# Kernel tuning notes

Hardware: AMD Instinct MI355X
Metric: run time of the kernel (lower is better)

## Reference

```python
import jax, jax.numpy as jnp
import numpy as np

N = 50000          # nodes
E = 800000         # directed edges (before self-loops)
HID = 64           # hidden_dim
HEADS = 4          # conv1 heads
NUM_CLASSES = 16
SLOPE = 0.2        # PyG GATConv default negative_slope


def setup_inputs() -> dict:
    key = jax.random.key(0)
    ks = jax.random.split(key, 10)
    s1 = 1.0 / np.sqrt(HID)
    s2 = 1.0 / np.sqrt(HEADS * HID)
    return {
        "x": jax.random.normal(ks[0], (N, HID), jnp.float32),
        "edge_index": jax.random.randint(ks[1], (2, E), 0, N, dtype=jnp.int64),
        # conv1: GATConv(64 -> 64, heads=4, concat)
        "W1": jax.random.normal(ks[2], (HID, HEADS * HID), jnp.float32) * s1,
        "att_src1": jax.random.normal(ks[3], (HEADS, HID), jnp.float32) * s1,
        "att_dst1": jax.random.normal(ks[4], (HEADS, HID), jnp.float32) * s1,
        "b1": jnp.zeros((HEADS * HID,), jnp.float32),
        # conv2: GATConv(256 -> num_classes, heads=1, concat)
        "W2": jax.random.normal(ks[5], (HEADS * HID, NUM_CLASSES), jnp.float32) * s2,
        "att_src2": jax.random.normal(ks[6], (1, NUM_CLASSES), jnp.float32) * s2,
        "att_dst2": jax.random.normal(ks[7], (1, NUM_CLASSES), jnp.float32) * s2,
        "b2": jnp.zeros((NUM_CLASSES,), jnp.float32),
    }


def _gat_conv(x, src, dst, W, att_s, att_d, b, heads, out_dim):
    # x: [N, F_in]; src/dst: [E'] with self-loops (PyG add_self_loops=True)
    xh = (x @ W).reshape(-1, heads, out_dim)                 # [N, H, D]
    a_src = jnp.einsum('nhd,hd->nh', xh, att_s)              # [N, H]
    a_dst = jnp.einsum('nhd,hd->nh', xh, att_d)              # [N, H]
    e = a_src[src] + a_dst[dst]                              # [E', H]
    e = jnp.where(e > 0, e, SLOPE * e)                       # leaky_relu(0.2)
    # segment softmax over incoming edges of each dst node
    m = jax.lax.stop_gradient(jax.ops.segment_max(e, dst, num_segments=N))
    ex = jnp.exp(e - m[dst])
    denom = jax.ops.segment_sum(ex, dst, num_segments=N)
    alpha = ex / (denom[dst] + 1e-16)                        # [E', H]
    out = jax.ops.segment_sum(xh[src] * alpha[:, :, None], dst, num_segments=N)
    return out.reshape(N, heads * out_dim) + b


def reference(x, edge_index, W1, att_src1, att_dst1, b1, W2, att_src2, att_dst2, b2):
    loops = jnp.arange(N, dtype=edge_index.dtype)
    src = jnp.concatenate([edge_index[0], loops])
    dst = jnp.concatenate([edge_index[1], loops])
    h = _gat_conv(x, src, dst, W1, att_src1, att_dst1, b1, HEADS, HID)
    h = jax.nn.elu(h)
    # F.dropout(p=0.5, training=False) -> identity at inference
    h = _gat_conv(h, src, dst, W2, att_src2, att_dst2, b2, 1, NUM_CLASSES)
    return jax.nn.log_softmax(h, axis=1)
```

## Files before the change

kernel.cpp:

```cpp
#include <hip/hip_runtime.h>
#include <hip/hip_bf16.h>
#include <math.h>

#define N_NODES 50000
#define N_EDGES 800000
#define EP (N_EDGES + N_NODES)
#define HID 64
#define HEADS 4
#define F1 (HEADS * HID)
#define NC 16
#define SLOPE 0.2f
#define NRT 3125
#define GMB 2048
#define NT 49

typedef __attribute__((ext_vector_type(8))) short short8;
typedef __attribute__((ext_vector_type(4))) float f32x4;

__device__ __forceinline__ unsigned short bf16rn(float f) {
    unsigned u = __float_as_uint(f);
    return (unsigned short)((u + 0x7fffu + ((u >> 16) & 1u)) >> 16);
}
__device__ __forceinline__ float bf_lo(unsigned p) { return __uint_as_float(p << 16); }
__device__ __forceinline__ float bf_hi(unsigned p) { return __uint_as_float(p & 0xffff0000u); }

__device__ __forceinline__ void edge_sd(int e, const int* __restrict__ ei, int& s, int& d) {
    if (e < N_EDGES) { s = ei[e]; d = ei[N_EDGES + e]; }
    else             { s = e - N_EDGES; d = s; }
}

__global__ __launch_bounds__(1024) void k_scan_local(const int* __restrict__ cnt,
        int* __restrict__ lexcl, int* __restrict__ bsum) {
    __shared__ int wsum[16];
    int t = threadIdx.x, lane = t & 63, wid = t >> 6;
    int i = blockIdx.x * 1024 + t;
    int v = (i < N_NODES) ? cnt[i] : 0;
    int s = v;
#pragma unroll
    for (int off = 1; off < 64; off <<= 1) {
        int x = __shfl_up(s, off);
        if (lane >= off) s += x;
    }
    if (lane == 63) wsum[wid] = s;
    __syncthreads();
    if (t < 16) {
        int w = wsum[t];
#pragma unroll
        for (int off = 1; off < 16; off <<= 1) {
            int x = __shfl_up(w, off);
            if (t >= off) w += x;
        }
        wsum[t] = w;
    }
    __syncthreads();
    int waveoff = (wid == 0) ? 0 : wsum[wid - 1];
    int incl = s + waveoff;
    if (i < N_NODES) lexcl[i] = incl - v;
    if (t == 1023) bsum[blockIdx.x] = incl;
}

__global__ __launch_bounds__(256) void k_scan_add(int* __restrict__ row_start,
        const int* __restrict__ bsum, int* __restrict__ cursor) {
    __shared__ int sb[64];
    __shared__ int stot;
    int t = threadIdx.x;
    if (t < 64) {
        int v = (t < NT) ? bsum[t] : 0;
        int s = v;
#pragma unroll
        for (int off = 1; off < 64; off <<= 1) {
            int x = __shfl_up(s, off);
            if (t >= off) s += x;
        }
        sb[t] = s - v;
        if (t == 63) stot = s;
    }
    __syncthreads();
    int i = blockIdx.x * 256 + t;
    if (i < N_NODES) {
        int v = row_start[i] + sb[i >> 10];
        row_start[i] = v;
        cursor[i] = v;
    }
    if (i == 0) row_start[N_NODES] = stot;
}

__global__ void k_scatter(const int* __restrict__ ei, int* __restrict__ cursor,
                          int* __restrict__ esrc) {
    int e = blockIdx.x * blockDim.x + threadIdx.x;
    if (e >= EP) return;
    int s, d; edge_sd(e, ei, s, d);
    int p = atomicAdd(&cursor[d], 1);
    esrc[p] = s;
}

__global__ __launch_bounds__(256) void k_gemm1(
        const float* __restrict__ x, const float* __restrict__ W1,
        const float* __restrict__ att_s, const float* __restrict__ att_d,
        unsigned short* __restrict__ xh1b, float* __restrict__ a_src, float* __restrict__ a_dst,
        const int* __restrict__ ei, int* __restrict__ cnt) {
    __shared__ float xs[16][68];
    int t = threadIdx.x;
    for (int e = blockIdx.x * 256 + t; e < EP; e += 256 * GMB) {
        int s, d; edge_sd(e, ei, s, d);
        atomicAdd(&cnt[d], 1);
    }
    int w = t >> 6, l = t & 63;
    int lo16 = l & 15, kg = l >> 4;
    short8 bfrag[4][2];
#pragma unroll
    for (int ct = 0; ct < 4; ++ct)
#pragma unroll
        for (int kh = 0; kh < 2; ++kh) {
            const float* wp = W1 + (size_t)(kh * 32 + kg * 8) * F1 + (w * 64 + ct * 16 + lo16);
            short8 f;
#pragma unroll
            for (int i = 0; i < 8; ++i) f[i] = (short)bf16rn(wp[(size_t)i * F1]);
            bfrag[ct][kh] = f;
        }
    float asv[4], adv[4];
#pragma unroll
    for (int ct = 0; ct < 4; ++ct) {
        asv[ct] = att_s[w * 64 + ct * 16 + lo16];
        adv[ct] = att_d[w * 64 + ct * 16 + lo16];
    }
    int sr = t >> 4, sc = (t & 15) * 4;
    for (int rt = blockIdx.x; rt < NRT; rt += GMB) {
        __syncthreads();
        *(float4*)&xs[sr][sc] = *(const float4*)(x + (size_t)(rt * 16 + sr) * HID + sc);
        __syncthreads();
        short8 af[2];
#pragma unroll
        for (int kh = 0; kh < 2; ++kh) {
            const float* xp = &xs[lo16][kh * 32 + kg * 8];
            float4 u0 = *(const float4*)xp;
            float4 u1 = *(const float4*)(xp + 4);
            short8 f;
            f[0] = (short)bf16rn(u0.x); f[1] = (short)bf16rn(u0.y);
            f[2] = (short)bf16rn(u0.z); f[3] = (short)bf16rn(u0.w);
            f[4] = (short)bf16rn(u1.x); f[5] = (short)bf16rn(u1.y);
            f[6] = (short)bf16rn(u1.z); f[7] = (short)bf16rn(u1.w);
            af[kh] = f;
        }
        f32x4 acc[4];
#pragma unroll
        for (int ct = 0; ct < 4; ++ct) {
            acc[ct] = (f32x4){0.f, 0.f, 0.f, 0.f};
            acc[ct] = __builtin_amdgcn_mfma_f32_16x16x32_bf16(af[0], bfrag[ct][0], acc[ct], 0, 0, 0);
            acc[ct] = __builtin_amdgcn_mfma_f32_16x16x32_bf16(af[1], bfrag[ct][1], acc[ct], 0, 0, 0);
        }
#pragma unroll
        for (int reg = 0; reg < 4; ++reg) {
            int gr = rt * 16 + kg * 4 + reg;
#pragma unroll
            for (int ct = 0; ct < 4; ++ct)
                xh1b[(size_t)gr * F1 + w * 64 + ct * 16 + lo16] = bf16rn(acc[ct][reg]);
            float ps = acc[0][reg] * asv[0] + acc[1][reg] * asv[1]
                     + acc[2][reg] * asv[2] + acc[3][reg] * asv[3];
            float pd = acc[0][reg] * adv[0] + acc[1][reg] * adv[1]
                     + acc[2][reg] * adv[2] + acc[3][reg] * adv[3];
#pragma unroll
            for (int o = 1; o <= 8; o <<= 1) {
                ps += __shfl_xor(ps, o);
                pd += __shfl_xor(pd, o);
            }
            if (lo16 == 0) {
                a_src[gr * HEADS + w] = ps;
                a_dst[gr * HEADS + w] = pd;
            }
        }
    }
}

__global__ __launch_bounds__(256) void k_csr1(
        const int* __restrict__ row_start, const int* __restrict__ esrc,
        const float* __restrict__ a_src, const float* __restrict__ a_dst,
        const unsigned short* __restrict__ xh1b, const float* __restrict__ b1,
        const float* __restrict__ W2, const float* __restrict__ att_s2,
        const float* __restrict__ att_d2,
        unsigned short* __restrict__ xh2b, float* __restrict__ a_src2,
        float* __restrict__ a_dst2) {
    int w = threadIdx.x >> 6, l = threadIdx.x & 63;
    int d = blockIdx.x * 4 + w;
    if (d >= N_NODES) return;
    int base = row_start[d], deg = row_start[d + 1] - base;
    __shared__ int   ls[4][64];
    __shared__ float lal[4][4][68];
    int h = l >> 4, e16 = l & 15;
    int eoff = l >> 5, fl = l & 31, hf = fl >> 3;
    int* lsw = ls[w];
    float adh = a_dst[d * HEADS + h];
    float denl = 0.0f;
    float a0=0.f,a1=0.f,a2=0.f,a3=0.f,a4=0.f,a5=0.f,a6=0.f,a7=0.f;
    for (int c0 = 0; c0 < deg; c0 += 64) {
        int cn = min(64, deg - c0);
        if (l < cn) lsw[l] = esrc[base + c0 + l];
        for (int j = e16; j < cn; j += 16) {
            float ev = a_src[lsw[j] * HEADS + h] + adh;
            ev = ev > 0.0f ? ev : SLOPE * ev;
            float wj = __expf(ev);
            lal[w][h][j] = wj;
            denl += wj;
        }
        const float* lalh = lal[w][hf];
        int j = 0;
        for (; j + 3 < cn; j += 4) {
            float wa = lalh[j + eoff], wb = lalh[j + 2 + eoff];
            uint4 pa = *(const uint4*)(xh1b + (size_t)lsw[j + eoff]     * F1 + 8 * fl);
            uint4 pb = *(const uint4*)(xh1b + (size_t)lsw[j + 2 + eoff] * F1 + 8 * fl);
            a0 += wa * bf_lo(pa.x); a1 += wa * bf_hi(pa.x);
            a2 += wa * bf_lo(pa.y); a3 += wa * bf_hi(pa.y);
            a4 += wa * bf_lo(pa.z); a5 += wa * bf_hi(pa.z);
            a6 += wa * bf_lo(pa.w); a7 += wa * bf_hi(pa.w);
            a0 += wb * bf_lo(pb.x); a1 += wb * bf_hi(pb.x);
            a2 += wb * bf_lo(pb.y); a3 += wb * bf_hi(pb.y);
            a4 += wb * bf_lo(pb.z); a5 += wb * bf_hi(pb.z);
            a6 += wb * bf_lo(pb.w); a7 += wb * bf_hi(pb.w);
        }
        for (; j + 1 < cn; j += 2) {
            float wa = lalh[j + eoff];
            uint4 pa = *(const uint4*)(xh1b + (size_t)lsw[j + eoff] * F1 + 8 * fl);
            a0 += wa * bf_lo(pa.x); a1 += wa * bf_hi(pa.x);
            a2 += wa * bf_lo(pa.y); a3 += wa * bf_hi(pa.y);
            a4 += wa * bf_lo(pa.z); a5 += wa * bf_hi(pa.z);
            a6 += wa * bf_lo(pa.w); a7 += wa * bf_hi(pa.w);
        }
        if (j < cn && eoff == 0) {
            float wa = lalh[j];
            uint4 pa = *(const uint4*)(xh1b + (size_t)lsw[j] * F1 + 8 * fl);
            a0 += wa * bf_lo(pa.x); a1 += wa * bf_hi(pa.x);
            a2 += wa * bf_lo(pa.y); a3 += wa * bf_hi(pa.y);
            a4 += wa * bf_lo(pa.z); a5 += wa * bf_hi(pa.z);
            a6 += wa * bf_lo(pa.w); a7 += wa * bf_hi(pa.w);
        }
    }
#pragma unroll
    for (int o = 8; o >= 1; o >>= 1) denl += __shfl_xor(denl, o);
    float dd = __shfl(denl, hf * 16);
    float inv = 1.0f / (dd + 1e-16f);
    a0 += __shfl_xor(a0, 32); a1 += __shfl_xor(a1, 32);
    a2 += __shfl_xor(a2, 32); a3 += __shfl_xor(a3, 32);
    a4 += __shfl_xor(a4, 32); a5 += __shfl_xor(a5, 32);
    a6 += __shfl_xor(a6, 32); a7 += __shfl_xor(a7, 32);
    float4 bb0 = *(const float4*)(b1 + 8 * fl);
    float4 bb1 = *(const float4*)(b1 + 8 * fl + 4);
    float v0 = a0 * inv + bb0.x, v1 = a1 * inv + bb0.y;
    float v2 = a2 * inv + bb0.z, v3 = a3 * inv + bb0.w;
    float v4 = a4 * inv + bb1.x, v5 = a5 * inv + bb1.y;
    float v6 = a6 * inv + bb1.z, v7 = a7 * inv + bb1.w;
    v0 = v0 > 0.0f ? v0 : (__expf(v0) - 1.0f);
    v1 = v1 > 0.0f ? v1 : (__expf(v1) - 1.0f);
    v2 = v2 > 0.0f ? v2 : (__expf(v2) - 1.0f);
    v3 = v3 > 0.0f ? v3 : (__expf(v3) - 1.0f);
    v4 = v4 > 0.0f ? v4 : (__expf(v4) - 1.0f);
    v5 = v5 > 0.0f ? v5 : (__expf(v5) - 1.0f);
    v6 = v6 > 0.0f ? v6 : (__expf(v6) - 1.0f);
    v7 = v7 > 0.0f ? v7 : (__expf(v7) - 1.0f);
    float* hrow = &lal[w][0][0];
    if (l < 32) {
        *(float4*)(hrow + 8 * fl)     = make_float4(v0, v1, v2, v3);
        *(float4*)(hrow + 8 * fl + 4) = make_float4(v4, v5, v6, v7);
    }
    int k0 = l >> 2;
    int cg = (l & 3) * 4;
    const float4* w4 = (const float4*)W2;
    float q0 = 0.0f, q1 = 0.0f, q2 = 0.0f, q3 = 0.0f;
#pragma unroll
    for (int j = 0; j < 16; ++j) {
        float hk = hrow[k0 + 16 * j];
        float4 wv = w4[l + 64 * j];
        q0 += hk * wv.x; q1 += hk * wv.y; q2 += hk * wv.z; q3 += hk * wv.w;
    }
#pragma unroll
    for (int o = 4; o <= 32; o <<= 1) {
        q0 += __shfl_xor(q0, o); q1 += __shfl_xor(q1, o);
        q2 += __shfl_xor(q2, o); q3 += __shfl_xor(q3, o);
    }
    if (l < 4) {
        unsigned u0 = (unsigned)bf16rn(q0) | ((unsigned)bf16rn(q1) << 16);
        unsigned u1 = (unsigned)bf16rn(q2) | ((unsigned)bf16rn(q3) << 16);
        *(uint2*)(xh2b + (size_t)d * NC + 4 * l) = make_uint2(u0, u1);
        float ps = q0 * att_s2[cg] + q1 * att_s2[cg + 1]
                 + q2 * att_s2[cg + 2] + q3 * att_s2[cg + 3];
        float pd = q0 * att_d2[cg] + q1 * att_d2[cg + 1]
                 + q2 * att_d2[cg + 2] + q3 * att_d2[cg + 3];
        ps += __shfl_xor(ps, 1); ps += __shfl_xor(ps, 2);
        pd += __shfl_xor(pd, 1); pd += __shfl_xor(pd, 2);
        if (l == 0) { a_src2[d] = ps; a_dst2[d] = pd; }
    }
}

__global__ __launch_bounds__(256) void k_csr2(
        const int* __restrict__ row_start, const int* __restrict__ esrc,
        const float* __restrict__ a_src2, const float* __restrict__ a_dst2,
        const unsigned short* __restrict__ xh2b, const float* __restrict__ b2,
        float* __restrict__ out) {
    int w = threadIdx.x >> 6, l = threadIdx.x & 63;
    int d = blockIdx.x * 4 + w;
    if (d >= N_NODES) return;
    int base = row_start[d], deg = row_start[d + 1] - base;
    __shared__ int   ls[4][64];
    __shared__ float lal[4][64];
    float adh = a_dst2[d];
    int cp4 = l & 3, je = l >> 2;
    float denl = 0.0f, a0 = 0.0f, a1 = 0.0f, a2 = 0.0f, a3 = 0.0f;
    for (int c0 = 0; c0 < deg; c0 += 64) {
        int cn = min(64, deg - c0);
        if (l < cn) {
            int s = esrc[base + c0 + l];
            ls[w][l] = s;
            float ev = a_src2[s] + adh;
            ev = ev > 0.0f ? ev : SLOPE * ev;
            float wj = __expf(ev);
            lal[w][l] = wj;
            denl += wj;
        }
        for (int j = je; j < cn; j += 16) {
            float wj = lal[w][j];
            uint2 pv = *(const uint2*)(xh2b + (size_t)ls[w][j] * NC + 4 * cp4);
            a0 += wj * bf_lo(pv.x); a1 += wj * bf_hi(pv.x);
            a2 += wj * bf_lo(pv.y); a3 += wj * bf_hi(pv.y);
        }
    }
#pragma unroll
    for (int o = 32; o >= 1; o >>= 1) denl += __shfl_xor(denl, o);
#pragma unroll
    for (int o = 4; o <= 32; o <<= 1) {
        a0 += __shfl_xor(a0, o); a1 += __shfl_xor(a1, o);
        a2 += __shfl_xor(a2, o); a3 += __shfl_xor(a3, o);
    }
    float inv = 1.0f / (denl + 1e-16f);
    float v0 = a0 * inv + b2[4 * cp4 + 0];
    float v1 = a1 * inv + b2[4 * cp4 + 1];
    float v2 = a2 * inv + b2[4 * cp4 + 2];
    float v3 = a3 * inv + b2[4 * cp4 + 3];
    float mm = fmaxf(fmaxf(v0, v1), fmaxf(v2, v3));
    mm = fmaxf(mm, __shfl_xor(mm, 1));
    mm = fmaxf(mm, __shfl_xor(mm, 2));
    float se = __expf(v0 - mm) + __expf(v1 - mm) + __expf(v2 - mm) + __expf(v3 - mm);
    se += __shfl_xor(se, 1);
    se += __shfl_xor(se, 2);
    float lse = mm + logf(se);
    if (l < 4) *(float4*)(out + (size_t)d * NC + 4 * l)
                   = make_float4(v0 - lse, v1 - lse, v2 - lse, v3 - lse);
}

extern "C" void kernel_launch(void* const* d_in, const int* in_sizes, int n_in,
                              void* d_out, int out_size, void* d_ws, size_t ws_size,
                              hipStream_t stream) {
    const float* x        = (const float*)d_in[0];
    const int*   ei       = (const int*)d_in[1];
    const float* W1       = (const float*)d_in[2];
    const float* att_src1 = (const float*)d_in[3];
    const float* att_dst1 = (const float*)d_in[4];
    const float* b1       = (const float*)d_in[5];
    const float* W2       = (const float*)d_in[6];
    const float* att_src2 = (const float*)d_in[7];
    const float* att_dst2 = (const float*)d_in[8];
    const float* b2       = (const float*)d_in[9];
    float* out = (float*)d_out;

    char* p = (char*)d_ws;
    unsigned short* xh1b  = (unsigned short*)p; p += (size_t)N_NODES * F1 * 2;
    unsigned short* xh2b  = (unsigned short*)p; p += (size_t)N_NODES * NC * 2;
    float* a_src1 = (float*)p; p += (size_t)N_NODES * HEADS * 4;
    float* a_dst1 = (float*)p; p += (size_t)N_NODES * HEADS * 4;
    float* a_src2 = (float*)p; p += (size_t)N_NODES * 4;
    float* a_dst2 = (float*)p; p += (size_t)N_NODES * 4;
    int* cnt       = (int*)p;  p += (size_t)N_NODES * 4;
    int* cursor    = (int*)p;  p += (size_t)N_NODES * 4;
    int* row_start = (int*)p;  p += (size_t)(N_NODES + 1) * 4;
    int* bsum      = (int*)p;  p += 64 * 4;
    int* esrc      = (int*)p;  p += (size_t)EP * 4;

    hipMemsetAsync(cnt, 0, (size_t)N_NODES * 4, stream);
    k_gemm1<<<GMB, 256, 0, stream>>>(x, W1, att_src1, att_dst1, xh1b, a_src1, a_dst1,
                                     ei, cnt);
    k_scan_local<<<NT, 1024, 0, stream>>>(cnt, row_start, bsum);
    k_scan_add<<<(N_NODES + 255) / 256, 256, 0, stream>>>(row_start, bsum, cursor);
    k_scatter<<<(EP + 255) / 256, 256, 0, stream>>>(ei, cursor, esrc);

    k_csr1<<<(N_NODES + 3) / 4, 256, 0, stream>>>(row_start, esrc, a_src1, a_dst1, xh1b, b1,
                                                  W2, att_src2, att_dst2, xh2b, a_src2, a_dst2);

    k_csr2<<<(N_NODES + 3) / 4, 256, 0, stream>>>(row_start, esrc, a_src2, a_dst2, xh2b, b2, out);
}
```

Baseline: 203.7 us.

## Fuse CSR scan and scatter kernels into one cooperative kernel with grid syncs

Replaces the three kernels for local scan, scan-add and edge scatter with a single cooperative kernel of 49 blocks that uses grid.sync between phases. This removes two kernel launch boundaries and their gaps. In exchange the scatter phase now runs on only 49 blocks of 1024 threads instead of thousands of blocks, which may reduce parallelism for the atomic-heavy scatter, and grid syncs add their own overhead.

Result: slower. 243.4 us (+19.5%).

```diff
diff --git a/kernel.cpp b/kernel.cpp
--- a/kernel.cpp
+++ b/kernel.cpp
@@ -1,5 +1,6 @@
 #include <hip/hip_runtime.h>
 #include <hip/hip_bf16.h>
+#include <hip/hip_cooperative_groups.h>
 #include <math.h>
 
 #define N_NODES 50000
@@ -29,8 +30,11 @@
     else             { s = e - N_EDGES; d = s; }
 }
 
-__global__ __launch_bounds__(1024) void k_scan_local(const int* __restrict__ cnt,
-        int* __restrict__ lexcl, int* __restrict__ bsum) {
+__global__ __launch_bounds__(1024) void k_csr_build(
+        const int* __restrict__ ei, const int* __restrict__ cnt,
+        int* __restrict__ row_start, int* __restrict__ cursor,
+        int* __restrict__ esrc, int* __restrict__ bsum) {
+    cooperative_groups::grid_group grid = cooperative_groups::this_grid();
     __shared__ int wsum[16];
     int t = threadIdx.x, lane = t & 63, wid = t >> 6;
     int i = blockIdx.x * 1024 + t;
@@ -55,43 +59,32 @@
     __syncthreads();
     int waveoff = (wid == 0) ? 0 : wsum[wid - 1];
     int incl = s + waveoff;
-    if (i < N_NODES) lexcl[i] = incl - v;
+    if (i < N_NODES) row_start[i] = incl - v;
     if (t == 1023) bsum[blockIdx.x] = incl;
-}
-
-__global__ __launch_bounds__(256) void k_scan_add(int* __restrict__ row_start,
-        const int* __restrict__ bsum, int* __restrict__ cursor) {
-    __shared__ int sb[64];
-    __shared__ int stot;
-    int t = threadIdx.x;
-    if (t < 64) {
-        int v = (t < NT) ? bsum[t] : 0;
-        int s = v;
+    grid.sync();
+    if (blockIdx.x == 0 && t < 64) {
+        int bv = (t < NT) ? bsum[t] : 0;
+        int bs = bv;
 #pragma unroll
         for (int off = 1; off < 64; off <<= 1) {
-            int x = __shfl_up(s, off);
-            if (t >= off) s += x;
-        }
-        sb[t] = s - v;
-        if (t == 63) stot = s;
-    }
-    __syncthreads();
-    int i = blockIdx.x * 256 + t;
+            int x = __shfl_up(bs, off);
+            if (t >= off) bs += x;
+        }
+        if (t < NT) bsum[t] = bs - bv;
+        if (t == 63) row_start[N_NODES] = bs;
+    }
+    grid.sync();
     if (i < N_NODES) {
-        int v = row_start[i] + sb[i >> 10];
-        row_start[i] = v;
-        cursor[i] = v;
-    }
-    if (i == 0) row_start[N_NODES] = stot;
-}
-
-__global__ void k_scatter(const int* __restrict__ ei, int* __restrict__ cursor,
-                          int* __restrict__ esrc) {
-    int e = blockIdx.x * blockDim.x + threadIdx.x;
-    if (e >= EP) return;
-    int s, d; edge_sd(e, ei, s, d);
-    int p = atomicAdd(&cursor[d], 1);
-    esrc[p] = s;
+        int vv = row_start[i] + bsum[i >> 10];
+        row_start[i] = vv;
+        cursor[i] = vv;
+    }
+    grid.sync();
+    for (int e = blockIdx.x * 1024 + t; e < EP; e += NT * 1024) {
+        int s2, d2; edge_sd(e, ei, s2, d2);
+        int p = atomicAdd(&cursor[d2], 1);
+        esrc[p] = s2;
+    }
 }
 
 __global__ __launch_bounds__(256) void k_gemm1(
@@ -376,9 +369,12 @@
     hipMemsetAsync(cnt, 0, (size_t)N_NODES * 4, stream);
     k_gemm1<<<GMB, 256, 0, stream>>>(x, W1, att_src1, att_dst1, xh1b, a_src1, a_dst1,
                                      ei, cnt);
-    k_scan_local<<<NT, 1024, 0, stream>>>(cnt, row_start, bsum);
-    k_scan_add<<<(N_NODES + 255) / 256, 256, 0, stream>>>(row_start, bsum, cursor);
-    k_scatter<<<(EP + 255) / 256, 256, 0, stream>>>(ei, cursor, esrc);
+    {
+        void* args[] = { (void*)&ei, (void*)&cnt, (void*)&row_start,
+                         (void*)&cursor, (void*)&esrc, (void*)&bsum };
+        hipLaunchCooperativeKernel((const void*)k_csr_build, dim3(NT), dim3(1024),
+                                   args, 0, stream);
+    }
 
     k_csr1<<<(N_NODES + 3) / 4, 256, 0, stream>>>(row_start, esrc, a_src1, a_dst1, xh1b, b1,
                                                   W2, att_src2, att_dst2, xh2b, a_src2, a_dst2);
```
